# Kernel optimization log

Measured on AMD Instinct MI355X. Metric: run time of the kernel, lower is better.

The kernel has to match this reference:

```python
import jax, jax.numpy as jnp
import numpy as np

N = 100000
E = 3200000
D_IN = 512
D_HID = 128
D_OUT = 4


def setup_inputs() -> dict:
    key = jax.random.key(0)
    k1, k2, k3, k4, k5, k6 = jax.random.split(key, 6)
    x = jax.random.normal(k1, (N, D_IN), dtype=jnp.float32)
    edge_index = jax.random.randint(k2, (2, E), 0, N, dtype=jnp.int64)
    # GCNConv params (Glorot-ish scale)
    W1 = jax.random.normal(k3, (D_IN, D_HID), dtype=jnp.float32) / np.sqrt(D_IN)
    b1 = jax.random.normal(k4, (D_HID,), dtype=jnp.float32) * 0.01
    W2 = jax.random.normal(k5, (D_HID, D_OUT), dtype=jnp.float32) / np.sqrt(D_HID)
    b2 = jax.random.normal(k6, (D_OUT,), dtype=jnp.float32) * 0.01
    return {"x": x, "edge_index": edge_index, "W1": W1, "b1": b1, "W2": W2, "b2": b2}


def _gcn_conv(x, W, b, src, dst, deg_inv_sqrt):
    # h = X W, then symmetric-normalized aggregation with self-loops (PyG GCNConv default)
    h = x @ W                                   # [N, F_out]
    norm = deg_inv_sqrt[src] * deg_inv_sqrt[dst]  # [E]
    agg = jax.ops.segment_sum(h[src] * norm[:, None], dst, num_segments=x.shape[0])
    # self-loop contribution: norm_ii = deg_inv_sqrt[i]^2
    agg = agg + h * (deg_inv_sqrt ** 2)[:, None]
    return agg + b


def reference(x, edge_index, W1, b1, W2, b2):
    src, dst = edge_index[0], edge_index[1]
    # degree with added self-loops (edge weights = 1)
    deg = jax.ops.segment_sum(jnp.ones((E,), dtype=x.dtype), dst, num_segments=N) + 1.0
    deg_inv_sqrt = jax.lax.rsqrt(deg)
    h = jax.nn.relu(_gcn_conv(x, W1, b1, src, dst, deg_inv_sqrt))
    out = _gcn_conv(h, W2, b2, src, dst, deg_inv_sqrt)
    return out
```

## Files before the change

kernel.cpp:

```cpp
#include <hip/hip_runtime.h>
#include <hip/hip_fp16.h>

#define DIN 512
#define DHID 128
#define DOUT 4
#define BSH 8
#define PA_CHUNK 8192

typedef _Float16 f16x8 __attribute__((ext_vector_type(8)));
typedef _Float16 f16x4 __attribute__((ext_vector_type(4)));
typedef float    f32x4 __attribute__((ext_vector_type(4)));

#define GLOAD_LDS(gp, lp)                                                     \
  __builtin_amdgcn_global_load_lds(                                           \
      (const __attribute__((address_space(1))) void*)(gp),                    \
      (__attribute__((address_space(3))) void*)(lp), 16, 0, 0)

__global__ void detect_i64_k(const int* __restrict__ raw, int* __restrict__ flag) {
  if (blockIdx.x == 0 && threadIdx.x == 0) {
    int z = 1;
    for (int k = 0; k < 8; ++k)
      if (raw[2 * k + 1] != 0) z = 0;
    flag[0] = z;
  }
}

__global__ __launch_bounds__(256) void bcount_k(const int* __restrict__ raw,
                                                const int* __restrict__ flag,
                                                int* __restrict__ gbcnt, int E) {
  __shared__ int h[512];
  const int tid = threadIdx.x;
  const int f = flag[0];
  for (int i = tid; i < 512; i += 256) h[i] = 0;
  __syncthreads();
  const size_t e0 = (size_t)blockIdx.x * PA_CHUNK;
  #pragma unroll
  for (int k = 0; k < 32; ++k) {
    size_t e = e0 + (size_t)k * 256 + tid;
    if (e < (size_t)E) {
      int d = f ? raw[2 * ((size_t)E + e)] : raw[(size_t)E + e];
      atomicAdd(&h[d >> BSH], 1);
    }
  }
  __syncthreads();
  for (int i = tid; i < 512; i += 256)
    if (h[i]) atomicAdd(&gbcnt[i], h[i]);
}

__global__ __launch_bounds__(512) void bscan_k(const int* __restrict__ gbcnt,
                                               int* __restrict__ boffs,
                                               int* __restrict__ bcur,
                                               int* __restrict__ offs,
                                               int nbkt, int N, int E) {
  __shared__ int sm[512];
  int t = threadIdx.x;
  int v = (t < nbkt) ? gbcnt[t] : 0;
  int x = v;
  sm[t] = x;
  __syncthreads();
  #pragma unroll
  for (int o = 1; o < 512; o <<= 1) {
    int y = (t >= o) ? sm[t - o] : 0;
    __syncthreads();
    x += y;
    sm[t] = x;
    __syncthreads();
  }
  if (t < nbkt) {
    boffs[t] = x - v;
    bcur[t] = x - v;
  }
  if (t == 0) {
    boffs[nbkt] = E;
    offs[N] = E;
  }
}

__global__ __launch_bounds__(256) void binA_k(const int* __restrict__ raw,
                                              const int* __restrict__ flag,
                                              int* __restrict__ bcur,
                                              unsigned* __restrict__ pairs, int E) {
  __shared__ int hist[512];
  __shared__ int base[512];
  const int tid = threadIdx.x;
  const int f = flag[0];
  const size_t e0 = (size_t)blockIdx.x * PA_CHUNK;
  for (int i = tid; i < 512; i += 256) hist[i] = 0;
  __syncthreads();
  int es[32], ed[32];
  #pragma unroll
  for (int k = 0; k < 32; ++k) {
    size_t e = e0 + (size_t)k * 256 + tid;
    if (e < (size_t)E) {
      es[k] = f ? raw[2 * e] : raw[e];
      ed[k] = f ? raw[2 * ((size_t)E + e)] : raw[(size_t)E + e];
      atomicAdd(&hist[ed[k] >> BSH], 1);
    } else {
      ed[k] = -1;
    }
  }
  __syncthreads();
  for (int i = tid; i < 512; i += 256) {
    int c = hist[i];
    base[i] = c ? atomicAdd(&bcur[i], c) : 0;
    hist[i] = 0;
  }
  __syncthreads();
  #pragma unroll
  for (int k = 0; k < 32; ++k) {
    if (ed[k] >= 0) {
      int b = ed[k] >> BSH;
      int pos = base[b] + atomicAdd(&hist[b], 1);
      pairs[pos] = ((unsigned)es[k] << 8) | ((unsigned)ed[k] & 255u);
    }
  }
}

__global__ __launch_bounds__(256) void binB_k(const unsigned* __restrict__ pairs,
                                              const int* __restrict__ boffs,
                                              int* __restrict__ csr,
                                              int* __restrict__ offs,
                                              float* __restrict__ dis, int N) {
  __shared__ int lcnt[256];
  __shared__ int sc[256];
  const int tid = threadIdx.x;
  const int n0 = blockIdx.x << BSH;
  const int lo = boffs[blockIdx.x];
  const int hi = boffs[blockIdx.x + 1];
  lcnt[tid] = 0;
  __syncthreads();
  for (int j = lo + tid; j < hi; j += 256) atomicAdd(&lcnt[(int)(pairs[j] & 255u)], 1);
  __syncthreads();
  int v = lcnt[tid];
  int x = v;
  sc[tid] = x;
  __syncthreads();
  #pragma unroll
  for (int o = 1; o < 256; o <<= 1) {
    int y = (tid >= o) ? sc[tid - o] : 0;
    __syncthreads();
    x += y;
    sc[tid] = x;
    __syncthreads();
  }
  const int base = lo + x - v;
  const int node = n0 + tid;
  if (node < N) {
    offs[node] = base;
    dis[node] = rsqrtf((float)v + 1.0f);
  }
  __syncthreads();
  lcnt[tid] = base;
  __syncthreads();
  for (int j = lo + tid; j < hi; j += 256) {
    unsigned p = pairs[j];
    int dl = (int)(p & 255u);
    int pos = atomicAdd(&lcnt[dl], 1);
    csr[pos] = (int)(p >> 8);
  }
}

__global__ __launch_bounds__(256) void wsplit_k(const float* __restrict__ W1,
                                                __half* __restrict__ Bt2) {
  int idx = blockIdx.x * 256 + threadIdx.x;
  if (idx >= DIN * DHID) return;
  int k = idx >> 7;
  int n = idx & 127;
  int kt = k >> 5, kk = k & 31;
  float w = W1[idx];
  _Float16 hi = (_Float16)w;
  _Float16 lo = (_Float16)(w - (float)hi);
  size_t base = (size_t)(kt * 128 + n) * 64;
  Bt2[base + kk]      = *(__half*)&hi;
  Bt2[base + 32 + kk] = *(__half*)&lo;
}

__global__ __launch_bounds__(256, 4) void gemm1_k(const float* __restrict__ A,
                                                  const __half* __restrict__ Bt2,
                                                  const float* __restrict__ dis,
                                                  __half* __restrict__ hs, int N) {
  __shared__ _Float16 smem[128 * 136];
  char* sAc = (char*)smem;
  char* sBc = (char*)smem + 16384;
  const int tid = threadIdx.x;
  const int wave = tid >> 6, lane = tid & 63;
  const int lr = lane & 15, quad = lane >> 4;
  const int m0 = blockIdx.x * 128;
  const int mbase = (wave >> 1) * 64;
  const int nbase = (wave & 1) * 64;
  const int wbase = (tid & ~63) * 16;

  f32x4 acc[4][4];
  #pragma unroll
  for (int mt = 0; mt < 4; ++mt)
    #pragma unroll
    for (int nt = 0; nt < 4; ++nt) acc[mt][nt] = (f32x4){0.f, 0.f, 0.f, 0.f};

  int arow[4], achk[4];
  #pragma unroll
  for (int l = 0; l < 4; ++l) {
    int d16 = l * 256 + tid;
    int row = d16 >> 3;
    arow[l] = row;
    achk[l] = (d16 & 7) ^ (row & 7);
  }

  for (int kt = 0; kt < 16; ++kt) {
    const int k0 = kt * 32;
    #pragma unroll
    for (int l = 0; l < 4; ++l) {
      int gr = m0 + arow[l];
      if (gr >= N) gr = N - 1;
      GLOAD_LDS(A + (size_t)gr * DIN + k0 + achk[l] * 4,
                sAc + (size_t)l * 4096 + wbase);
    }
    #pragma unroll
    for (int l = 0; l < 4; ++l) {
      GLOAD_LDS(Bt2 + (size_t)(kt * 128 + arow[l]) * 64 + achk[l] * 8,
                sBc + (size_t)l * 4096 + wbase);
    }
    __syncthreads();
    f16x8 ah[4], al[4];
    #pragma unroll
    for (int mt = 0; mt < 4; ++mt) {
      int r = mbase + mt * 16 + lr;
      f32x4 v0 = *(const f32x4*)(sAc + r * 128 + (((2 * quad + 0) ^ (r & 7)) << 4));
      f32x4 v1 = *(const f32x4*)(sAc + r * 128 + (((2 * quad + 1) ^ (r & 7)) << 4));
      _Float16 c0 = (_Float16)v0[0], c1 = (_Float16)v0[1],
               c2 = (_Float16)v0[2], c3 = (_Float16)v0[3],
               c4 = (_Float16)v1[0], c5 = (_Float16)v1[1],
               c6 = (_Float16)v1[2], c7 = (_Float16)v1[3];
      ah[mt] = (f16x8){c0, c1, c2, c3, c4, c5, c6, c7};
      al[mt] = (f16x8){(_Float16)(v0[0] - (float)c0), (_Float16)(v0[1] - (float)c1),
                       (_Float16)(v0[2] - (float)c2), (_Float16)(v0[3] - (float)c3),
                       (_Float16)(v1[0] - (float)c4), (_Float16)(v1[1] - (float)c5),
                       (_Float16)(v1[2] - (float)c6), (_Float16)(v1[3] - (float)c7)};
    }
    #pragma unroll
    for (int nt = 0; nt < 4; ++nt) {
      int c = nbase + nt * 16 + lr;
      f16x8 bh = *(const f16x8*)(sBc + c * 128 + (((0 + quad) ^ (c & 7)) << 4));
      f16x8 bl = *(const f16x8*)(sBc + c * 128 + (((4 + quad) ^ (c & 7)) << 4));
      #pragma unroll
      for (int mt = 0; mt < 4; ++mt)
        acc[mt][nt] = __builtin_amdgcn_mfma_f32_16x16x32_f16(al[mt], bh, acc[mt][nt], 0, 0, 0);
      #pragma unroll
      for (int mt = 0; mt < 4; ++mt)
        acc[mt][nt] = __builtin_amdgcn_mfma_f32_16x16x32_f16(ah[mt], bl, acc[mt][nt], 0, 0, 0);
      #pragma unroll
      for (int mt = 0; mt < 4; ++mt)
        acc[mt][nt] = __builtin_amdgcn_mfma_f32_16x16x32_f16(ah[mt], bh, acc[mt][nt], 0, 0, 0);
    }
    __syncthreads();
  }
  #pragma unroll
  for (int mt = 0; mt < 4; ++mt) {
    #pragma unroll
    for (int r = 0; r < 4; ++r) {
      int row = mbase + mt * 16 + quad * 4 + r;
      int gr = m0 + row;
      float dv = dis[gr < N ? gr : (N - 1)];
      #pragma unroll
      for (int nt = 0; nt < 4; ++nt) {
        int col = nbase + nt * 16 + lr;
        smem[row * 136 + col] = (_Float16)(acc[mt][nt][r] * dv);
      }
    }
  }
  __syncthreads();
  #pragma unroll
  for (int l = 0; l < 8; ++l) {
    int idx = l * 256 + tid;
    int row = idx >> 4;
    int c = (idx & 15) << 3;
    int gr = m0 + row;
    if (gr < N)
      *(uint4*)(hs + (size_t)gr * DHID + c) = *(uint4*)&smem[row * 136 + c];
  }
}

__global__ __launch_bounds__(256) void agg1_k(const __half* __restrict__ hs,
                                              const float* __restrict__ dis,
                                              const int* __restrict__ offs,
                                              const int* __restrict__ csr,
                                              const float* __restrict__ W2,
                                              const float* __restrict__ b1,
                                              float* __restrict__ gs, int N) {
  const int wid = threadIdx.x >> 6;
  const int lane = threadIdx.x & 63;
  const int i = blockIdx.x * 4 + wid;
  if (i >= N) return;
  const int f = lane * 2;
  const __half* hp = hs + f;
  float ax = 0.f, ay = 0.f;
  const int beg = offs[i], end = offs[i + 1];
  for (int base = beg; base < end; base += 64) {
    int sj = 0;
    if (base + lane < end) sj = csr[base + lane];
    const int n = min(64, end - base);
    int t = 0;
    for (; t + 8 <= n; t += 8) {
      int s0 = __shfl(sj, t + 0, 64), s1 = __shfl(sj, t + 1, 64);
      int s2 = __shfl(sj, t + 2, 64), s3 = __shfl(sj, t + 3, 64);
      int s4 = __shfl(sj, t + 4, 64), s5 = __shfl(sj, t + 5, 64);
      int s6 = __shfl(sj, t + 6, 64), s7 = __shfl(sj, t + 7, 64);
      __half2 h0 = *(const __half2*)(hp + (size_t)s0 * DHID);
      __half2 h1 = *(const __half2*)(hp + (size_t)s1 * DHID);
      __half2 h2 = *(const __half2*)(hp + (size_t)s2 * DHID);
      __half2 h3 = *(const __half2*)(hp + (size_t)s3 * DHID);
      __half2 h4 = *(const __half2*)(hp + (size_t)s4 * DHID);
      __half2 h5 = *(const __half2*)(hp + (size_t)s5 * DHID);
      __half2 h6 = *(const __half2*)(hp + (size_t)s6 * DHID);
      __half2 h7 = *(const __half2*)(hp + (size_t)s7 * DHID);
      float2 f0 = __half22float2(h0), f1 = __half22float2(h1);
      float2 f2 = __half22float2(h2), f3 = __half22float2(h3);
      float2 f4 = __half22float2(h4), f5 = __half22float2(h5);
      float2 f6 = __half22float2(h6), f7 = __half22float2(h7);
      ax += ((f0.x + f1.x) + (f2.x + f3.x)) + ((f4.x + f5.x) + (f6.x + f7.x));
      ay += ((f0.y + f1.y) + (f2.y + f3.y)) + ((f4.y + f5.y) + (f6.y + f7.y));
    }
    for (; t < n; ++t) {
      int s = __shfl(sj, t, 64);
      float2 hf = __half22float2(*(const __half2*)(hp + (size_t)s * DHID));
      ax += hf.x;
      ay += hf.y;
    }
  }
  {
    float2 hf = __half22float2(*(const __half2*)(hp + (size_t)i * DHID));
    ax += hf.x;
    ay += hf.y;
  }
  const float di = dis[i];
  float v0 = fmaxf(fmaf(ax, di, b1[f]), 0.f);
  float v1 = fmaxf(fmaf(ay, di, b1[f + 1]), 0.f);
  float p0 = fmaf(v0, W2[f * 4 + 0], v1 * W2[f * 4 + 4]);
  float p1 = fmaf(v0, W2[f * 4 + 1], v1 * W2[f * 4 + 5]);
  float p2 = fmaf(v0, W2[f * 4 + 2], v1 * W2[f * 4 + 6]);
  float p3 = fmaf(v0, W2[f * 4 + 3], v1 * W2[f * 4 + 7]);
  #pragma unroll
  for (int o = 32; o > 0; o >>= 1) {
    p0 += __shfl_xor(p0, o, 64);
    p1 += __shfl_xor(p1, o, 64);
    p2 += __shfl_xor(p2, o, 64);
    p3 += __shfl_xor(p3, o, 64);
  }
  if (lane == 0)
    *(float4*)(gs + (size_t)i * DOUT) = make_float4(p0 * di, p1 * di, p2 * di, p3 * di);
}

__global__ __launch_bounds__(256) void agg2_k(const float* __restrict__ gs,
                                              const float* __restrict__ dis,
                                              const int* __restrict__ offs,
                                              const int* __restrict__ csr,
                                              const float* __restrict__ b2,
                                              float* __restrict__ out, int N) {
  int i = blockIdx.x * 256 + threadIdx.x;
  if (i >= N) return;
  float a0 = 0.f, a1 = 0.f, a2 = 0.f, a3 = 0.f;
  const int beg = offs[i], end = offs[i + 1];
  int j = beg;
  for (; j + 4 <= end; j += 4) {
    int s0 = csr[j], s1 = csr[j + 1], s2 = csr[j + 2], s3 = csr[j + 3];
    float4 g0 = *(const float4*)(gs + (size_t)s0 * DOUT);
    float4 g1 = *(const float4*)(gs + (size_t)s1 * DOUT);
    float4 g2 = *(const float4*)(gs + (size_t)s2 * DOUT);
    float4 g3 = *(const float4*)(gs + (size_t)s3 * DOUT);
    a0 += (g0.x + g1.x) + (g2.x + g3.x);
    a1 += (g0.y + g1.y) + (g2.y + g3.y);
    a2 += (g0.z + g1.z) + (g2.z + g3.z);
    a3 += (g0.w + g1.w) + (g2.w + g3.w);
  }
  for (; j < end; ++j) {
    int s = csr[j];
    float4 gv = *(const float4*)(gs + (size_t)s * DOUT);
    a0 += gv.x; a1 += gv.y; a2 += gv.z; a3 += gv.w;
  }
  const float di = dis[i];
  float4 gi = *(const float4*)(gs + (size_t)i * DOUT);
  float4 o4;
  o4.x = fmaf(a0 + gi.x, di, b2[0]);
  o4.y = fmaf(a1 + gi.y, di, b2[1]);
  o4.z = fmaf(a2 + gi.z, di, b2[2]);
  o4.w = fmaf(a3 + gi.w, di, b2[3]);
  *(float4*)(out + (size_t)i * DOUT) = o4;
}

extern "C" void kernel_launch(void* const* d_in, const int* in_sizes, int n_in,
                              void* d_out, int out_size, void* d_ws, size_t ws_size,
                              hipStream_t stream) {
  const float* x  = (const float*)d_in[0];
  const int*   raw = (const int*)d_in[1];
  const float* W1 = (const float*)d_in[2];
  const float* b1 = (const float*)d_in[3];
  const float* W2 = (const float*)d_in[4];
  const float* b2 = (const float*)d_in[5];
  float* out = (float*)d_out;

  const int N = in_sizes[0] / DIN;
  const int E = in_sizes[1] / 2;

  char* ws = (char*)d_ws;
  size_t off = 0;
  auto carve = [&](size_t bytes) -> char* {
    char* p = ws + off;
    off = (off + bytes + 255) & ~(size_t)255;
    return p;
  };
  float*    dis  = (float*)carve((size_t)N * 4);
  int*      offs = (int*)carve((size_t)(N + 1) * 4);
  int*      csr  = (int*)carve((size_t)E * 4);
  unsigned* pairs= (unsigned*)carve((size_t)E * 4);
  int*      boffs= (int*)carve(513 * 4);
  int*      bcur = (int*)carve(512 * 4);
  int*      gbcnt= (int*)carve(512 * 4);
  int*      flag = (int*)carve(256);
  __half*   Bt2  = (__half*)carve((size_t)DIN * DHID * 2 * 2);
  __half*   hs   = (__half*)carve((size_t)N * DHID * 2);
  float*    gs   = (float*)carve((size_t)N * DOUT * 4);
  (void)ws_size; (void)n_in; (void)out_size;

  const int gN = (N + 255) / 256;
  const int nbkt = (N + (1 << BSH) - 1) >> BSH;
  const int gA = (E + PA_CHUNK - 1) / PA_CHUNK;

  detect_i64_k<<<1, 64, 0, stream>>>(raw, flag);
  hipMemsetAsync(gbcnt, 0, 512 * 4, stream);
  bcount_k<<<gA, 256, 0, stream>>>(raw, flag, gbcnt, E);
  bscan_k<<<1, 512, 0, stream>>>(gbcnt, boffs, bcur, offs, nbkt, N, E);
  binA_k<<<gA, 256, 0, stream>>>(raw, flag, bcur, pairs, E);
  binB_k<<<nbkt, 256, 0, stream>>>(pairs, boffs, csr, offs, dis, N);
  wsplit_k<<<(DIN * DHID + 255) / 256, 256, 0, stream>>>(W1, Bt2);
  gemm1_k<<<(N + 127) / 128, 256, 0, stream>>>(x, Bt2, dis, hs, N);
  agg1_k<<<(N + 3) / 4, 256, 0, stream>>>(hs, dis, offs, csr, W2, b1, gs, N);
  agg2_k<<<gN, 256, 0, stream>>>(gs, dis, offs, csr, b2, out, N);
}
```

Measured before the change: 535.3 us.

## Double-buffer A tile in gemm1 and prefetch next K-slice during MFMA

The first-layer GEMM kernel now double-buffers the fp32 A tile in LDS and issues global-to-LDS loads for the next K slice before computing the current one. It waits with explicit vmcnt counters and raw s_barrier instead of __syncthreads. The B tile stays single-buffered and is reloaded after a barrier at the end of each iteration. Shared memory grows to 48 KB and the occupancy hint drops from 4 to 2 blocks per CU, trading occupancy for hiding load latency behind compute.

```diff
diff --git a/kernel.cpp b/kernel.cpp
--- a/kernel.cpp
+++ b/kernel.cpp
@@ -175,13 +175,12 @@
   Bt2[base + 32 + kk] = *(__half*)&lo;
 }
 
-__global__ __launch_bounds__(256, 4) void gemm1_k(const float* __restrict__ A,
+__global__ __launch_bounds__(256, 2) void gemm1_k(const float* __restrict__ A,
                                                   const __half* __restrict__ Bt2,
                                                   const float* __restrict__ dis,
                                                   __half* __restrict__ hs, int N) {
-  __shared__ _Float16 smem[128 * 136];
-  char* sAc = (char*)smem;
-  char* sBc = (char*)smem + 16384;
+  __shared__ char smem[49152];
+  char* const sB = smem + 32768;
   const int tid = threadIdx.x;
   const int wave = tid >> 6, lane = tid & 63;
   const int lr = lane & 15, quad = lane >> 4;
@@ -196,36 +195,46 @@
     #pragma unroll
     for (int nt = 0; nt < 4; ++nt) acc[mt][nt] = (f32x4){0.f, 0.f, 0.f, 0.f};
 
-  int arow[4], achk[4];
+  const float*  agp[4];
+  const __half* bgp[4];
   #pragma unroll
   for (int l = 0; l < 4; ++l) {
     int d16 = l * 256 + tid;
     int row = d16 >> 3;
-    arow[l] = row;
-    achk[l] = (d16 & 7) ^ (row & 7);
-  }
-
+    int chk = (d16 & 7) ^ (row & 7);
+    int gr = m0 + row;
+    if (gr >= N) gr = N - 1;
+    agp[l] = A + (size_t)gr * DIN + chk * 4;
+    bgp[l] = Bt2 + (size_t)row * 64 + chk * 8;
+  }
+
+  #pragma unroll
+  for (int l = 0; l < 4; ++l)
+    GLOAD_LDS(agp[l], smem + l * 4096 + wbase);
+  #pragma unroll
+  for (int l = 0; l < 4; ++l)
+    GLOAD_LDS(bgp[l], sB + l * 4096 + wbase);
+
+  int cur = 0;
   for (int kt = 0; kt < 16; ++kt) {
-    const int k0 = kt * 32;
-    #pragma unroll
-    for (int l = 0; l < 4; ++l) {
-      int gr = m0 + arow[l];
-      if (gr >= N) gr = N - 1;
-      GLOAD_LDS(A + (size_t)gr * DIN + k0 + achk[l] * 4,
-                sAc + (size_t)l * 4096 + wbase);
-    }
-    #pragma unroll
-    for (int l = 0; l < 4; ++l) {
-      GLOAD_LDS(Bt2 + (size_t)(kt * 128 + arow[l]) * 64 + achk[l] * 8,
-                sBc + (size_t)l * 4096 + wbase);
-    }
-    __syncthreads();
+    if (kt < 15) {
+      char* dA = smem + (cur ^ 1) * 16384;
+      #pragma unroll
+      for (int l = 0; l < 4; ++l)
+        GLOAD_LDS(agp[l] + (kt + 1) * 32, dA + l * 4096 + wbase);
+      asm volatile("s_waitcnt vmcnt(4)" ::: "memory");
+    } else {
+      asm volatile("s_waitcnt vmcnt(0)" ::: "memory");
+    }
+    __builtin_amdgcn_s_barrier();
+    asm volatile("" ::: "memory");
+    char* sA = smem + cur * 16384;
     f16x8 ah[4], al[4];
     #pragma unroll
     for (int mt = 0; mt < 4; ++mt) {
       int r = mbase + mt * 16 + lr;
-      f32x4 v0 = *(const f32x4*)(sAc + r * 128 + (((2 * quad + 0) ^ (r & 7)) << 4));
-      f32x4 v1 = *(const f32x4*)(sAc + r * 128 + (((2 * quad + 1) ^ (r & 7)) << 4));
+      f32x4 v0 = *(const f32x4*)(sA + r * 128 + (((2 * quad + 0) ^ (r & 7)) << 4));
+      f32x4 v1 = *(const f32x4*)(sA + r * 128 + (((2 * quad + 1) ^ (r & 7)) << 4));
       _Float16 c0 = (_Float16)v0[0], c1 = (_Float16)v0[1],
                c2 = (_Float16)v0[2], c3 = (_Float16)v0[3],
                c4 = (_Float16)v1[0], c5 = (_Float16)v1[1],
@@ -239,8 +248,8 @@
     #pragma unroll
     for (int nt = 0; nt < 4; ++nt) {
       int c = nbase + nt * 16 + lr;
-      f16x8 bh = *(const f16x8*)(sBc + c * 128 + (((0 + quad) ^ (c & 7)) << 4));
-      f16x8 bl = *(const f16x8*)(sBc + c * 128 + (((4 + quad) ^ (c & 7)) << 4));
+      f16x8 bh = *(const f16x8*)(sB + c * 128 + (((0 + quad) ^ (c & 7)) << 4));
+      f16x8 bl = *(const f16x8*)(sB + c * 128 + (((4 + quad) ^ (c & 7)) << 4));
       #pragma unroll
       for (int mt = 0; mt < 4; ++mt)
         acc[mt][nt] = __builtin_amdgcn_mfma_f32_16x16x32_f16(al[mt], bh, acc[mt][nt], 0, 0, 0);
@@ -251,8 +260,17 @@
       for (int mt = 0; mt < 4; ++mt)
         acc[mt][nt] = __builtin_amdgcn_mfma_f32_16x16x32_f16(ah[mt], bh, acc[mt][nt], 0, 0, 0);
     }
-    __syncthreads();
-  }
+    __builtin_amdgcn_sched_barrier(0);
+    __builtin_amdgcn_s_barrier();
+    asm volatile("" ::: "memory");
+    if (kt < 15) {
+      #pragma unroll
+      for (int l = 0; l < 4; ++l)
+        GLOAD_LDS(bgp[l] + (size_t)(kt + 1) * 8192, sB + l * 4096 + wbase);
+    }
+    cur ^= 1;
+  }
+  _Float16* sep = (_Float16*)smem;
   #pragma unroll
   for (int mt = 0; mt < 4; ++mt) {
     #pragma unroll
@@ -263,7 +281,7 @@
       #pragma unroll
       for (int nt = 0; nt < 4; ++nt) {
         int col = nbase + nt * 16 + lr;
-        smem[row * 136 + col] = (_Float16)(acc[mt][nt][r] * dv);
+        sep[row * 136 + col] = (_Float16)(acc[mt][nt][r] * dv);
       }
     }
   }
@@ -275,7 +293,7 @@
     int c = (idx & 15) << 3;
     int gr = m0 + row;
     if (gr < N)
-      *(uint4*)(hs + (size_t)gr * DHID + c) = *(uint4*)&smem[row * 136 + c];
+      *(uint4*)(hs + (size_t)gr * DHID + c) = *(uint4*)&sep[row * 136 + c];
   }
 }
 
```

Result: no change. 533.1 us (-0.4%).
